# Optimization experiments

Hardware: AMD Instinct MI355X
Metric: run time of the kernel (lower is better)

Reference implementation:

```python
import jax, jax.numpy as jnp
import numpy as np

B, A, N, FIN, H, HEADS, OUT = 32, 64, 121, 12, 128, 4, 256
NL = 2          # transformer encoder layers
LEVELS = 4      # complete ternary tree: N = (3**(LEVELS+1)-1)//2 = 121
EPS = 1e-5


def setup_inputs() -> dict:
    key = jax.random.key(0)
    ks = jax.random.split(key, 10)
    s = 0.02
    # adjacency: complete ternary tree, local node indices, rows [parent, child, branch]
    child = np.arange(1, N)
    parent = (child - 1) // 3
    branch = (child - 1) % 3
    adj = np.stack([parent, child, branch], -1).astype(np.int32)  # (N-1, 3)
    adjacency = jnp.asarray(np.broadcast_to(adj, (B, A, N - 1, 3)).copy())
    perm = jax.random.permutation(ks[0], N)  # torch.randperm(n_nodes) equivalent
    forest = jax.random.normal(ks[1], (B, A, N, FIN), jnp.float32)
    p = lambda k, shape: s * jax.random.normal(k, shape, jnp.float32)
    return dict(
        forest=forest, adjacency=adjacency, perm=perm,
        w_in=p(ks[2], (H, FIN)), b_in=jnp.zeros((H,), jnp.float32),
        qkv_w=p(ks[3], (NL, 3 * H, H)), qkv_b=jnp.zeros((NL, 3 * H), jnp.float32),
        proj_w=p(ks[4], (NL, H, H)), proj_b=jnp.zeros((NL, H), jnp.float32),
        ff1_w=p(ks[5], (NL, H, H)), ff1_b=jnp.zeros((NL, H), jnp.float32),
        ff2_w=p(ks[6], (NL, H, H)), ff2_b=jnp.zeros((NL, H), jnp.float32),
        ln1_g=jnp.ones((NL, H), jnp.float32), ln1_b=jnp.zeros((NL, H), jnp.float32),
        ln2_g=jnp.ones((NL, H), jnp.float32), ln2_b=jnp.zeros((NL, H), jnp.float32),
        w_out=p(ks[7], (OUT, N * H)), b_out=jnp.zeros((OUT,), jnp.float32),
        lnf_g=jnp.ones((OUT,), jnp.float32), lnf_b=jnp.zeros((OUT,), jnp.float32))


def _ln(x, g, b):
    m = x.mean(-1, keepdims=True)
    v = ((x - m) ** 2).mean(-1, keepdims=True)  # biased var, as torch LayerNorm
    return (x - m) * jax.lax.rsqrt(v + EPS) * g + b


def _tree_pe(adjacency):
    """Level-parallel tree positional encoding: pe[child] = pe[parent] with
    bit (depth*3 + branch) set to 1 (depth 0 = first level below root)."""
    parent = adjacency[..., 0]
    branch = adjacency[..., 2]
    pe = jnp.zeros((B, A, N, H), jnp.float32)
    for l in range(1, LEVELS + 1):
        s0 = (3 ** l - 1) // 2          # first node index at level l
        e0 = (3 ** (l + 1) - 1) // 2    # one past last node at level l
        pa = parent[..., s0 - 1:e0 - 1]             # (B, A, n_l) parent local idx
        br = branch[..., s0 - 1:e0 - 1]             # (B, A, n_l) branch 0/1/2
        ppe = jnp.take_along_axis(pe, pa[..., None], axis=2)  # gather parent PE
        bits = jax.nn.one_hot((l - 1) * 3 + br, H, dtype=jnp.float32)
        pe = pe.at[:, :, s0:e0, :].set(ppe + bits)
    return pe


def _mha(x, wqkv, bqkv, wo, bo):
    S = x.shape[0]
    hd = H // HEADS
    qkv = x @ wqkv.T + bqkv
    q, k, v = [t.reshape(S, N, HEADS, hd) for t in jnp.split(qkv, 3, axis=-1)]
    logits = jnp.einsum('bqhd,bkhd->bhqk', q, k) / float(np.sqrt(hd))
    o = jnp.einsum('bhqk,bkhd->bqhd', jax.nn.softmax(logits, -1), v)
    return o.reshape(S, N, H) @ wo.T + bo


def _forward(forest, adjacency, perm, w_in, b_in, qkv_w, qkv_b, proj_w, proj_b,
             ff1_w, ff1_b, ff2_w, ff2_b, ln1_g, ln1_b, ln2_g, ln2_b,
             w_out, b_out, lnf_g, lnf_b):
    x = forest @ w_in.T + b_in + _tree_pe(adjacency)        # (B, A, N, H)
    x = x.reshape(B * A, N, H)[:, perm]                      # token shuffle
    for i in range(NL):  # post-norm encoder layers, relu FFN, dropout=0
        x = _ln(x + _mha(x, qkv_w[i], qkv_b[i], proj_w[i], proj_b[i]), ln1_g[i], ln1_b[i])
        h = jnp.maximum(x @ ff1_w[i].T + ff1_b[i], 0.0)
        x = _ln(x + h @ ff2_w[i].T + ff2_b[i], ln2_g[i], ln2_b[i])
    y = x.reshape(B * A, N * H) @ w_out.T + b_out
    return _ln(y.reshape(B, A, OUT), lnf_g, lnf_b)


def reference(forest, adjacency, perm, w_in, b_in, qkv_w, qkv_b, proj_w, proj_b,
              ff1_w, ff1_b, ff2_w, ff2_b, ln1_g, ln1_b, ln2_g, ln2_b,
              w_out, b_out, lnf_g, lnf_b):
    return _forward(forest, adjacency, perm, w_in, b_in, qkv_w, qkv_b, proj_w, proj_b,
                    ff1_w, ff1_b, ff2_w, ff2_b, ln1_g, ln1_b, ln2_g, ln2_b,
                    w_out, b_out, lnf_g, lnf_b)
```

## Files before the change

### kernel.cpp

```cpp
#include <hip/hip_runtime.h>


typedef unsigned short u16;
typedef __attribute__((ext_vector_type(8))) short bf16x8;
typedef __attribute__((ext_vector_type(4))) float f32x4;
typedef __attribute__((ext_vector_type(4))) unsigned int u32x4;

#define NTOK 121
#define HD 128
#define S_TOT 2048
#define EPSF 1e-5f

__device__ inline u16 f2bf(float f) {
  unsigned u = __float_as_uint(f);
  return (u16)((u + 0x7FFFu + ((u >> 16) & 1u)) >> 16);
}
__device__ inline float bf2f(u16 h) { return __uint_as_float(((unsigned)h) << 16); }

__device__ inline f32x4 mfma16(bf16x8 a, bf16x8 b, f32x4 c) {
  return __builtin_amdgcn_mfma_f32_16x16x32_bf16(a, b, c, 0, 0, 0);
}

__device__ inline unsigned cvt_pk_bf16(float lo, float hi) {
  unsigned r;
  asm("v_cvt_pk_bf16_f32 %0, %1, %2" : "=v"(r) : "v"(lo), "v"(hi));
  return r;
}

__device__ inline f32x4 vmax4(f32x4 a, f32x4 b) {
  f32x4 r;
  r[0] = fmaxf(a[0], b[0]); r[1] = fmaxf(a[1], b[1]);
  r[2] = fmaxf(a[2], b[2]); r[3] = fmaxf(a[3], b[3]);
  return r;
}

__device__ inline void stage16(const void* g, void* l) {
  __builtin_amdgcn_global_load_lds((__attribute__((address_space(1))) void*)g,
                                   (__attribute__((address_space(3))) void*)l,
                                   16, 0, 0);
}

__device__ inline void quad_repack(unsigned pkA, unsigned pkB, int quad,
                                   unsigned& mlo, unsigned& mhi) {
  unsigned y = (quad < 2) ? pkA : pkB;
  unsigned z = (quad < 2) ? pkB : pkA;
  unsigned a16 = (unsigned)__shfl_xor((int)y, 16);
  unsigned a32 = (unsigned)__shfl_xor((int)z, 32);
  unsigned a48 = (unsigned)__shfl_xor((int)z, 48);
  mlo = (quad == 0) ? y   : (quad == 1) ? a48 : (quad == 2) ? a32 : a16;
  mhi = (quad == 0) ? a16 : (quad == 1) ? a32 : (quad == 2) ? a48 : y;
}

__global__ __launch_bounds__(256) void convw_kernel(
    const float* __restrict__ qkvw, const float* __restrict__ projw,
    const float* __restrict__ ff1w, const float* __restrict__ ff2w,
    const float* __restrict__ wout, u16* __restrict__ dst) {
  int i = blockIdx.x * 256 + threadIdx.x;
  float v;
  if (i < 98304) v = qkvw[i];
  else if (i < 131072) v = projw[i - 98304];
  else if (i < 163840) v = ff1w[i - 131072];
  else if (i < 196608) v = ff2w[i - 163840];
  else v = wout[i - 196608];
  dst[i] = f2bf(v);
}

__global__ __launch_bounds__(256) void inproj_kernel(
    const float* __restrict__ forest, const int* __restrict__ adj,
    const int* __restrict__ perm, const float* __restrict__ WIN,
    const float* __restrict__ BIN, u16* __restrict__ X) {
  __shared__ float wf[128 * 12];
  __shared__ float fr[121 * 12];
  __shared__ float pe[121 * 12];
  __shared__ int pm[121];
  int s = blockIdx.x, tid = threadIdx.x;
  const float* fg = forest + (size_t)s * (NTOK * 12);
  const int* ag = adj + (size_t)s * (120 * 3);
  for (int i = tid; i < 128 * 12; i += 256) wf[i] = WIN[i];
  for (int i = tid; i < 121 * 12; i += 256) { fr[i] = fg[i]; pe[i] = 0.f; }
  if (tid < 121) pm[tid] = perm[tid];
  __syncthreads();
  if (tid > 0 && tid < 121) {
    int n = tid;
    int l = (n <= 3) ? 1 : (n <= 12) ? 2 : (n <= 39) ? 3 : 4;
    int cur = n;
    while (cur > 0) {
      int par = ag[(cur - 1) * 3];
      int br = ag[(cur - 1) * 3 + 2];
      pe[n * 12 + (l - 1) * 3 + br] = 1.f;
      cur = par; l--;
    }
  }
  __syncthreads();
  int h = tid & 127;
  for (int base = 0; base < 121; base += 2) {
    int i = base + (tid >> 7);
    if (i < 121) {
      int node = pm[i];
      float v = BIN[h];
#pragma unroll
      for (int k = 0; k < 12; ++k) v += fr[node * 12 + k] * wf[h * 12 + k];
      if (h < 12) v += pe[node * 12 + h];
      X[(size_t)s * (NTOK * HD) + i * HD + h] = f2bf(v);
    }
  }
}

__global__ __launch_bounds__(256, 2) void attn_kernel(
    const u16* __restrict__ X, u16* __restrict__ O,
    const u16* __restrict__ WQKV, const float* __restrict__ QKVB, int layer) {
  __shared__ u16 lds[16384];
  __shared__ u16 xl[15872];
  int tid = threadIdx.x;
  int wave = tid >> 6, lane = tid & 63, l16 = lane & 15, quad = lane >> 4;
  int seq = blockIdx.x >> 1;
  int head = ((blockIdx.x & 1) << 1) | (wave >> 1);
  int half = wave & 1;
  int hs = wave >> 1;
  u16* Kh = lds + hs * 4096;
  u16* Vh = lds + 8192 + hs * 4096;
  const u16* Xs = X + (size_t)seq * (NTOK * HD);
  const f32x4 fz = {0.f, 0.f, 0.f, 0.f};
  const int wbase = layer * 384 + head * 32;
  const u16* WQ = WQKV + (size_t)wbase * HD;
  const u16* WK = WQKV + (size_t)(wbase + 128) * HD;
  const u16* WV = WQKV + (size_t)(wbase + 256) * HD;

  {
    const char* Xb = (const char*)Xs;
#pragma unroll
    for (int j = 0; j < 8; ++j) {
      int i = wave * 8 + j;
      if (i < 31) {
        int n = i * 64 + lane;
        int r = n >> 4, c = n & 15;
        int rc = r > 120 ? 120 : r;
        stage16(Xb + rc * 256 + ((c ^ (r & 7)) << 4), (void*)(xl + i * 512));
      }
    }
  }
  bf16x8 wqf[2][4], wkf[2][4], wvf[2][4];
#pragma unroll
  for (int nt = 0; nt < 2; ++nt)
#pragma unroll
    for (int k = 0; k < 4; ++k) {
      size_t off = (size_t)(nt * 16 + l16) * HD + k * 32 + quad * 8;
      wqf[nt][k] = *(const bf16x8*)(WQ + off);
      wkf[nt][k] = *(const bf16x8*)(WK + off);
      wvf[nt][k] = *(const bf16x8*)(WV + off);
    }
  float kb2[2], vb2[2];
#pragma unroll
  for (int nt = 0; nt < 2; ++nt) {
    kb2[nt] = QKVB[wbase + 128 + nt * 16 + l16];
    vb2[nt] = QKVB[wbase + 256 + nt * 16 + l16];
  }
  const float scl = 0.17677669529663687f * 1.4426950408889634f;
  float qbias[2][4];
#pragma unroll
  for (int nt = 0; nt < 2; ++nt)
#pragma unroll
    for (int r = 0; r < 4; ++r)
      qbias[nt][r] = QKVB[wbase + nt * 16 + quad * 4 + r];
  asm volatile("s_waitcnt vmcnt(0)" ::: "memory");
  __syncthreads();

#pragma unroll 1
  for (int mt = 0; mt < 4; ++mt) {
    int tb = half * 64 + mt * 16;
    int arow = tb + l16; if (arow > 120) arow = 120;
    bf16x8 a[4];
#pragma unroll
    for (int k = 0; k < 4; ++k)
      a[k] = *(const bf16x8*)(xl + arow * 128 + (((k * 4 + quad) ^ (arow & 7)) << 3));
#pragma unroll
    for (int nt = 0; nt < 2; ++nt) {
      f32x4 kacc = fz, vacc = fz;
#pragma unroll
      for (int k = 0; k < 4; ++k) {
        kacc = mfma16(a[k], wkf[nt][k], kacc);
        vacc = mfma16(a[k], wvf[nt][k], vacc);
      }
      int d = nt * 16 + l16;
      int kc = nt * 2 + (l16 >> 3);
#pragma unroll
      for (int r = 0; r < 4; ++r) {
        int t = tb + quad * 4 + r;
        Kh[t * 32 + ((kc ^ (t & 3)) << 3) + (l16 & 7)] = f2bf(kacc[r] + kb2[nt]);
        float vv = (t < NTOK) ? (vacc[r] + vb2[nt]) : 0.f;
        Vh[d * 128 + (((t >> 3) ^ l16) << 3) + (t & 7)] = f2bf(vv);
      }
    }
  }
  __syncthreads();

#pragma unroll 1
  for (int qmt = 0; qmt < 4; ++qmt) {
    int qb = (half * 4 + qmt) * 16;
    int qrow = qb + l16;
    int qrowc = qrow > 120 ? 120 : qrow;
    bf16x8 xb[4];
#pragma unroll
    for (int k = 0; k < 4; ++k)
      xb[k] = *(const bf16x8*)(xl + qrowc * 128 + (((k * 4 + quad) ^ (qrowc & 7)) << 3));
    f32x4 qv[2];
#pragma unroll
    for (int nt = 0; nt < 2; ++nt) {
      f32x4 acc = fz;
#pragma unroll
      for (int k = 0; k < 4; ++k) acc = mfma16(wqf[nt][k], xb[k], acc);
      qv[nt] = acc;
    }
    unsigned qpk[2][2];
#pragma unroll
    for (int nt = 0; nt < 2; ++nt)
#pragma unroll
      for (int r2 = 0; r2 < 2; ++r2)
        qpk[nt][r2] = cvt_pk_bf16((qv[nt][2 * r2] + qbias[nt][2 * r2]) * scl,
                                  (qv[nt][2 * r2 + 1] + qbias[nt][2 * r2 + 1]) * scl);
    u32x4 qu;
#pragma unroll
    for (int r2 = 0; r2 < 2; ++r2) {
      unsigned mlo, mhi;
      quad_repack(qpk[0][r2], qpk[1][r2], quad, mlo, mhi);
      qu[r2] = mlo; qu[2 + r2] = mhi;
    }
    bf16x8 qfrag = __builtin_bit_cast(bf16x8, qu);
    f32x4 lg[8];
#pragma unroll
    for (int nt = 0; nt < 8; ++nt) {
      bf16x8 ka = *(const bf16x8*)(Kh + (nt * 16 + l16) * 32 + ((quad ^ (l16 & 3)) << 3));
      lg[nt] = mfma16(ka, qfrag, fz);
    }
    f32x4 t0 = vmax4(vmax4(lg[0], lg[1]), vmax4(lg[2], lg[3]));
    f32x4 t1 = vmax4(vmax4(lg[4], lg[5]), vmax4(lg[6], lg[7]));
    f32x4 tm = vmax4(t0, t1);
    float mx = fmaxf(fmaxf(tm[0], tm[1]), fmaxf(tm[2], tm[3]));
    mx = fmaxf(mx, __shfl_xor(mx, 16));
    mx = fmaxf(mx, __shfl_xor(mx, 32));
#pragma unroll
    for (int nt = 0; nt < 8; ++nt)
#pragma unroll
      for (int r = 0; r < 4; ++r) {
        float ev = __builtin_amdgcn_exp2f(lg[nt][r] - mx);
        if (nt == 7 && (quad * 4 + r > 8)) ev = 0.f;
        lg[nt][r] = ev;
      }
    f32x4 s4 = (lg[0] + lg[1]) + (lg[2] + lg[3]) + ((lg[4] + lg[5]) + (lg[6] + lg[7]));
    float sum = (s4[0] + s4[1]) + (s4[2] + s4[3]);
    sum += __shfl_xor(sum, 16);
    sum += __shfl_xor(sum, 32);
    float rinv = __builtin_amdgcn_rcpf(sum);
    unsigned pk[8][2];
#pragma unroll
    for (int nt = 0; nt < 8; ++nt)
#pragma unroll
      for (int r2 = 0; r2 < 2; ++r2)
        pk[nt][r2] = cvt_pk_bf16(lg[nt][2 * r2], lg[nt][2 * r2 + 1]);
    f32x4 oacc[2] = {fz, fz};
#pragma unroll
    for (int s = 0; s < 4; ++s) {
      u32x4 pu;
#pragma unroll
      for (int r2 = 0; r2 < 2; ++r2) {
        unsigned mlo, mhi;
        quad_repack(pk[2 * s][r2], pk[2 * s + 1][r2], quad, mlo, mhi);
        pu[r2] = mlo; pu[2 + r2] = mhi;
      }
      bf16x8 pfrag = __builtin_bit_cast(bf16x8, pu);
#pragma unroll
      for (int mt = 0; mt < 2; ++mt) {
        bf16x8 va = *(const bf16x8*)(Vh + (mt * 16 + l16) * 128 + (((s * 4 + quad) ^ l16) << 3));
        oacc[mt] = mfma16(va, pfrag, oacc[mt]);
      }
    }
    if (qrow < NTOK) {
      u16* Op = O + (size_t)seq * (NTOK * HD) + (size_t)qrow * HD + head * 32;
#pragma unroll
      for (int mt = 0; mt < 2; ++mt)
#pragma unroll
        for (int r2 = 0; r2 < 2; ++r2) {
          unsigned w = cvt_pk_bf16(oacc[mt][2 * r2] * rinv, oacc[mt][2 * r2 + 1] * rinv);
          *(unsigned*)(Op + mt * 16 + quad * 4 + 2 * r2) = w;
        }
    }
  }
}

__global__ __launch_bounds__(256) void projln_kernel(
    u16* __restrict__ X, const u16* __restrict__ O,
    const u16* __restrict__ WP, const float* __restrict__ PB,
    const float* __restrict__ G, const float* __restrict__ Bt, int layer) {
  __shared__ u16 as_[32 * 136];
  __shared__ float ct[32 * 132];
  int r0 = blockIdx.x * 32, tid = threadIdx.x;
  int wave = tid >> 6, lane = tid & 63, l16 = lane & 15, quad = lane >> 4;
  const f32x4 fz = {0.f, 0.f, 0.f, 0.f};
  for (int c = tid; c < 32 * 16; c += 256) {
    int row = c >> 4, g = c & 15;
    *(uint4*)(as_ + row * 136 + g * 8) = *(const uint4*)(O + (size_t)(r0 + row) * HD + g * 8);
  }
  __syncthreads();
  f32x4 acc[2][2] = {{fz, fz}, {fz, fz}};
#pragma unroll
  for (int k = 0; k < 4; ++k) {
    bf16x8 a0 = *(const bf16x8*)(as_ + l16 * 136 + k * 32 + quad * 8);
    bf16x8 a1 = *(const bf16x8*)(as_ + (16 + l16) * 136 + k * 32 + quad * 8);
#pragma unroll
    for (int n = 0; n < 2; ++n) {
      int nt = wave * 2 + n;
      bf16x8 bf = *(const bf16x8*)(WP + ((size_t)(layer * 128 + nt * 16 + l16)) * HD + k * 32 + quad * 8);
      acc[0][n] = mfma16(a0, bf, acc[0][n]);
      acc[1][n] = mfma16(a1, bf, acc[1][n]);
    }
  }
  for (int mt = 0; mt < 2; ++mt)
    for (int n = 0; n < 2; ++n) {
      int nt = wave * 2 + n;
#pragma unroll
      for (int r = 0; r < 4; ++r)
        ct[(mt * 16 + quad * 4 + r) * 132 + nt * 16 + l16] = acc[mt][n][r];
    }
  __syncthreads();
  int row = tid >> 3, l8 = tid & 7;
  size_t R = (size_t)(r0 + row);
  float v[16], sum = 0.f, ssq = 0.f;
#pragma unroll
  for (int i = 0; i < 16; ++i) {
    int c = l8 * 16 + i;
    float t = ct[row * 132 + c] + PB[layer * 128 + c] + bf2f(X[R * HD + c]);
    v[i] = t; sum += t; ssq += t * t;
  }
  for (int m = 1; m <= 4; m <<= 1) { sum += __shfl_xor(sum, m, 64); ssq += __shfl_xor(ssq, m, 64); }
  float mean = sum * (1.f / 128.f);
  float var = ssq * (1.f / 128.f) - mean * mean;
  float rstd = rsqrtf(var + EPSF);
#pragma unroll
  for (int i = 0; i < 16; ++i) {
    int c = l8 * 16 + i;
    X[R * HD + c] = f2bf((v[i] - mean) * rstd * G[layer * 128 + c] + Bt[layer * 128 + c]);
  }
}

__global__ __launch_bounds__(256) void ffn_kernel(
    u16* __restrict__ X,
    const u16* __restrict__ W1, const float* __restrict__ B1,
    const u16* __restrict__ W2, const float* __restrict__ B2,
    const float* __restrict__ G, const float* __restrict__ Bt, int layer) {
  __shared__ u16 as_[32 * 136];
  __shared__ u16 hs[32 * 136];
  __shared__ float ct[32 * 132];
  int r0 = blockIdx.x * 32, tid = threadIdx.x;
  int wave = tid >> 6, lane = tid & 63, l16 = lane & 15, quad = lane >> 4;
  const f32x4 fz = {0.f, 0.f, 0.f, 0.f};
  for (int c = tid; c < 32 * 16; c += 256) {
    int row = c >> 4, g = c & 15;
    *(uint4*)(as_ + row * 136 + g * 8) = *(const uint4*)(X + (size_t)(r0 + row) * HD + g * 8);
  }
  __syncthreads();
  f32x4 acc[2][2] = {{fz, fz}, {fz, fz}};
#pragma unroll
  for (int k = 0; k < 4; ++k) {
    bf16x8 a0 = *(const bf16x8*)(as_ + l16 * 136 + k * 32 + quad * 8);
    bf16x8 a1 = *(const bf16x8*)(as_ + (16 + l16) * 136 + k * 32 + quad * 8);
#pragma unroll
    for (int n = 0; n < 2; ++n) {
      int nt = wave * 2 + n;
      bf16x8 bf = *(const bf16x8*)(W1 + ((size_t)(layer * 128 + nt * 16 + l16)) * HD + k * 32 + quad * 8);
      acc[0][n] = mfma16(a0, bf, acc[0][n]);
      acc[1][n] = mfma16(a1, bf, acc[1][n]);
    }
  }
  for (int mt = 0; mt < 2; ++mt)
    for (int n = 0; n < 2; ++n) {
      int nt = wave * 2 + n;
      int col = nt * 16 + l16;
      float b1 = B1[layer * 128 + col];
#pragma unroll
      for (int r = 0; r < 4; ++r)
        hs[(mt * 16 + quad * 4 + r) * 136 + col] = f2bf(fmaxf(acc[mt][n][r] + b1, 0.f));
    }
  __syncthreads();
  f32x4 acc2[2][2] = {{fz, fz}, {fz, fz}};
#pragma unroll
  for (int k = 0; k < 4; ++k) {
    bf16x8 a0 = *(const bf16x8*)(hs + l16 * 136 + k * 32 + quad * 8);
    bf16x8 a1 = *(const bf16x8*)(hs + (16 + l16) * 136 + k * 32 + quad * 8);
#pragma unroll
    for (int n = 0; n < 2; ++n) {
      int nt = wave * 2 + n;
      bf16x8 bf = *(const bf16x8*)(W2 + ((size_t)(layer * 128 + nt * 16 + l16)) * HD + k * 32 + quad * 8);
      acc2[0][n] = mfma16(a0, bf, acc2[0][n]);
      acc2[1][n] = mfma16(a1, bf, acc2[1][n]);
    }
  }
  for (int mt = 0; mt < 2; ++mt)
    for (int n = 0; n < 2; ++n) {
      int nt = wave * 2 + n;
#pragma unroll
      for (int r = 0; r < 4; ++r)
        ct[(mt * 16 + quad * 4 + r) * 132 + nt * 16 + l16] = acc2[mt][n][r];
    }
  __syncthreads();
  int row = tid >> 3, l8 = tid & 7;
  size_t R = (size_t)(r0 + row);
  float v[16], sum = 0.f, ssq = 0.f;
#pragma unroll
  for (int i = 0; i < 16; ++i) {
    int c = l8 * 16 + i;
    float t = ct[row * 132 + c] + B2[layer * 128 + c] + bf2f(as_[row * 136 + c]);
    v[i] = t; sum += t; ssq += t * t;
  }
  for (int m = 1; m <= 4; m <<= 1) { sum += __shfl_xor(sum, m, 64); ssq += __shfl_xor(ssq, m, 64); }
  float mean = sum * (1.f / 128.f);
  float var = ssq * (1.f / 128.f) - mean * mean;
  float rstd = rsqrtf(var + EPSF);
#pragma unroll
  for (int i = 0; i < 16; ++i) {
    int c = l8 * 16 + i;
    X[R * HD + c] = f2bf((v[i] - mean) * rstd * G[layer * 128 + c] + Bt[layer * 128 + c]);
  }
}

__global__ __launch_bounds__(256, 2) void outgemm_kernel(
    const u16* __restrict__ X, const u16* __restrict__ WO, float* __restrict__ PART) {
  __shared__ u16 as_[64 * 136];
  int mtile = blockIdx.x, j = blockIdx.y;
  int tid = threadIdx.x, wave = tid >> 6, lane = tid & 63, l16 = lane & 15, quad = lane >> 4;
  int s0 = mtile * 64;
  int k0 = (j * 484) / 16, k1 = ((j + 1) * 484) / 16;
  const f32x4 fz = {0.f, 0.f, 0.f, 0.f};
  f32x4 acc[4][4];
  for (int a = 0; a < 4; ++a) for (int b = 0; b < 4; ++b) acc[a][b] = fz;
  for (int kb = k0; kb < k1; kb += 4) {
    int nst = (k1 - kb < 4) ? (k1 - kb) : 4;
    __syncthreads();
    int chunks = 64 * 4 * nst;
    for (int c = tid; c < chunks; c += 256) {
      int row = c / (4 * nst), g = c % (4 * nst);
      *(uint4*)(as_ + row * 136 + g * 8) =
          *(const uint4*)(X + (size_t)(s0 + row) * 15488 + kb * 32 + g * 8);
    }
    __syncthreads();
    for (int kk = 0; kk < nst; ++kk) {
      bf16x8 af[4];
#pragma unroll
      for (int mt = 0; mt < 4; ++mt)
        af[mt] = *(const bf16x8*)(as_ + (mt * 16 + l16) * 136 + kk * 32 + quad * 8);
#pragma unroll
      for (int n = 0; n < 4; ++n) {
        int nt = wave * 4 + n;
        bf16x8 bf = *(const bf16x8*)(WO + (size_t)(nt * 16 + l16) * 15488 +
                                     (size_t)(kb + kk) * 32 + quad * 8);
#pragma unroll
        for (int mt = 0; mt < 4; ++mt) acc[mt][n] = mfma16(af[mt], bf, acc[mt][n]);
      }
    }
  }
  for (int mt = 0; mt < 4; ++mt)
    for (int n = 0; n < 4; ++n) {
      int nt = wave * 4 + n;
#pragma unroll
      for (int r = 0; r < 4; ++r) {
        int row = s0 + mt * 16 + quad * 4 + r;
        PART[((size_t)j * 2048 + row) * 256 + nt * 16 + l16] = acc[mt][n][r];
      }
    }
}

__global__ __launch_bounds__(256) void lnf_kernel(
    const float* __restrict__ PART, const float* __restrict__ BO,
    const float* __restrict__ G, const float* __restrict__ Bt, float* __restrict__ OUT) {
  int s = blockIdx.x * 4 + (threadIdx.x >> 6);
  int lane = threadIdx.x & 63;
  float v[4], sum = 0.f, ssq = 0.f;
#pragma unroll
  for (int i = 0; i < 4; ++i) {
    int c = lane + i * 64;
    float t = BO[c];
    for (int jj = 0; jj < 16; ++jj) t += PART[((size_t)jj * 2048 + s) * 256 + c];
    v[i] = t; sum += t; ssq += t * t;
  }
  for (int m = 1; m <= 32; m <<= 1) { sum += __shfl_xor(sum, m, 64); ssq += __shfl_xor(ssq, m, 64); }
  float mean = sum * (1.f / 256.f);
  float var = ssq * (1.f / 256.f) - mean * mean;
  float rstd = rsqrtf(var + EPSF);
#pragma unroll
  for (int i = 0; i < 4; ++i) {
    int c = lane + i * 64;
    OUT[(size_t)s * 256 + c] = (v[i] - mean) * rstd * G[c] + Bt[c];
  }
}

extern "C" void kernel_launch(void* const* d_in, const int* in_sizes, int n_in,
                              void* d_out, int out_size, void* d_ws, size_t ws_size,
                              hipStream_t stream) {
  const float* forest = (const float*)d_in[0];
  const int* adj      = (const int*)d_in[1];
  const int* perm     = (const int*)d_in[2];
  const float* w_in   = (const float*)d_in[3];
  const float* b_in   = (const float*)d_in[4];
  const float* qkv_w  = (const float*)d_in[5];
  const float* qkv_b  = (const float*)d_in[6];
  const float* proj_w = (const float*)d_in[7];
  const float* proj_b = (const float*)d_in[8];
  const float* ff1_w  = (const float*)d_in[9];
  const float* ff1_b  = (const float*)d_in[10];
  const float* ff2_w  = (const float*)d_in[11];
  const float* ff2_b  = (const float*)d_in[12];
  const float* ln1_g  = (const float*)d_in[13];
  const float* ln1_b  = (const float*)d_in[14];
  const float* ln2_g  = (const float*)d_in[15];
  const float* ln2_b  = (const float*)d_in[16];
  const float* w_out  = (const float*)d_in[17];
  const float* b_out  = (const float*)d_in[18];
  const float* lnf_g  = (const float*)d_in[19];
  const float* lnf_b  = (const float*)d_in[20];

  char* ws = (char*)d_ws;
  u16* WB = (u16*)ws;
  u16* X  = (u16*)(ws + 8323072);
  u16* O  = (u16*)(ws + 8323072 + 63438848);
  float* PART = (float*)(ws + 8323072 + 2 * (size_t)63438848);

  u16* WQKV  = WB;
  u16* WPROJ = WB + 98304;
  u16* WFF1  = WB + 131072;
  u16* WFF2  = WB + 163840;
  u16* WOUT  = WB + 196608;

  convw_kernel<<<16256, 256, 0, stream>>>(qkv_w, proj_w, ff1_w, ff2_w, w_out, WB);
  inproj_kernel<<<2048, 256, 0, stream>>>(forest, adj, perm, w_in, b_in, X);
  for (int layer = 0; layer < 2; ++layer) {
    attn_kernel<<<4096, 256, 0, stream>>>(X, O, WQKV, qkv_b, layer);
    projln_kernel<<<7744, 256, 0, stream>>>(X, O, WPROJ, proj_b, ln1_g, ln1_b, layer);
    ffn_kernel<<<7744, 256, 0, stream>>>(X, WFF1, ff1_b, WFF2, ff2_b, ln2_g, ln2_b, layer);
  }
  outgemm_kernel<<<dim3(32, 16), 256, 0, stream>>>(X, WOUT, PART);
  lnf_kernel<<<512, 256, 0, stream>>>(PART, b_out, lnf_g, lnf_b, (float*)d_out);
}
```

Before: 718.5 us.

## Fuse projection+LN1 and FFN+LN2 into one register-resident block kernel

Merges the separate proj+layernorm and FFN+layernorm kernels into a single kernel handling 128 tokens per block. Each wave keeps two 16-token tiles in registers across all three GEMMs, repacking accumulators into MFMA operand fragments instead of round-tripping through shared memory or global X. This removes one launch and one global read/write of X per layer. It also adds s_setprio around MFMA groups in attention and vectorizes V and O stores. The cost is heavy register pressure from the 8x2 accumulator arrays, and weights are reloaded from global memory by every wave.

Result: faster. 689.5 us (-4.0%).

```diff
diff --git a/kernel.cpp b/kernel.cpp
--- a/kernel.cpp
+++ b/kernel.cpp
@@ -5,6 +5,7 @@
 typedef __attribute__((ext_vector_type(8))) short bf16x8;
 typedef __attribute__((ext_vector_type(4))) float f32x4;
 typedef __attribute__((ext_vector_type(4))) unsigned int u32x4;
+typedef __attribute__((ext_vector_type(2))) unsigned int u32x2;
 
 #define NTOK 121
 #define HD 128
@@ -16,6 +17,8 @@
   return (u16)((u + 0x7FFFu + ((u >> 16) & 1u)) >> 16);
 }
 __device__ inline float bf2f(u16 h) { return __uint_as_float(((unsigned)h) << 16); }
+__device__ inline float bfu32lo(unsigned u) { return __uint_as_float(u << 16); }
+__device__ inline float bfu32hi(unsigned u) { return __uint_as_float(u & 0xffff0000u); }
 
 __device__ inline f32x4 mfma16(bf16x8 a, bf16x8 b, f32x4 c) {
   return __builtin_amdgcn_mfma_f32_16x16x32_bf16(a, b, c, 0, 0, 0);
@@ -176,20 +179,28 @@
 #pragma unroll
     for (int nt = 0; nt < 2; ++nt) {
       f32x4 kacc = fz, vacc = fz;
+      __builtin_amdgcn_s_setprio(1);
 #pragma unroll
       for (int k = 0; k < 4; ++k) {
         kacc = mfma16(a[k], wkf[nt][k], kacc);
         vacc = mfma16(a[k], wvf[nt][k], vacc);
       }
+      __builtin_amdgcn_s_setprio(0);
       int d = nt * 16 + l16;
       int kc = nt * 2 + (l16 >> 3);
 #pragma unroll
       for (int r = 0; r < 4; ++r) {
         int t = tb + quad * 4 + r;
         Kh[t * 32 + ((kc ^ (t & 3)) << 3) + (l16 & 7)] = f2bf(kacc[r] + kb2[nt]);
-        float vv = (t < NTOK) ? (vacc[r] + vb2[nt]) : 0.f;
-        Vh[d * 128 + (((t >> 3) ^ l16) << 3) + (t & 7)] = f2bf(vv);
-      }
+      }
+      float vv[4];
+#pragma unroll
+      for (int r = 0; r < 4; ++r) {
+        int t = tb + quad * 4 + r;
+        vv[r] = (t < NTOK) ? (vacc[r] + vb2[nt]) : 0.f;
+      }
+      u32x2 vp = { cvt_pk_bf16(vv[0], vv[1]), cvt_pk_bf16(vv[2], vv[3]) };
+      *(u32x2*)(Vh + d * 128 + ((((tb >> 3) + (quad >> 1)) ^ l16) << 3) + (quad & 1) * 4) = vp;
     }
   }
   __syncthreads();
@@ -204,6 +215,7 @@
     for (int k = 0; k < 4; ++k)
       xb[k] = *(const bf16x8*)(xl + qrowc * 128 + (((k * 4 + quad) ^ (qrowc & 7)) << 3));
     f32x4 qv[2];
+    __builtin_amdgcn_s_setprio(1);
 #pragma unroll
     for (int nt = 0; nt < 2; ++nt) {
       f32x4 acc = fz;
@@ -211,6 +223,7 @@
       for (int k = 0; k < 4; ++k) acc = mfma16(wqf[nt][k], xb[k], acc);
       qv[nt] = acc;
     }
+    __builtin_amdgcn_s_setprio(0);
     unsigned qpk[2][2];
 #pragma unroll
     for (int nt = 0; nt < 2; ++nt)
@@ -227,11 +240,13 @@
     }
     bf16x8 qfrag = __builtin_bit_cast(bf16x8, qu);
     f32x4 lg[8];
+    __builtin_amdgcn_s_setprio(1);
 #pragma unroll
     for (int nt = 0; nt < 8; ++nt) {
       bf16x8 ka = *(const bf16x8*)(Kh + (nt * 16 + l16) * 32 + ((quad ^ (l16 & 3)) << 3));
       lg[nt] = mfma16(ka, qfrag, fz);
     }
+    __builtin_amdgcn_s_setprio(0);
     f32x4 t0 = vmax4(vmax4(lg[0], lg[1]), vmax4(lg[2], lg[3]));
     f32x4 t1 = vmax4(vmax4(lg[4], lg[5]), vmax4(lg[6], lg[7]));
     f32x4 tm = vmax4(t0, t1);
@@ -268,157 +283,227 @@
         pu[r2] = mlo; pu[2 + r2] = mhi;
       }
       bf16x8 pfrag = __builtin_bit_cast(bf16x8, pu);
+      __builtin_amdgcn_s_setprio(1);
 #pragma unroll
       for (int mt = 0; mt < 2; ++mt) {
         bf16x8 va = *(const bf16x8*)(Vh + (mt * 16 + l16) * 128 + (((s * 4 + quad) ^ l16) << 3));
         oacc[mt] = mfma16(va, pfrag, oacc[mt]);
       }
+      __builtin_amdgcn_s_setprio(0);
     }
     if (qrow < NTOK) {
       u16* Op = O + (size_t)seq * (NTOK * HD) + (size_t)qrow * HD + head * 32;
 #pragma unroll
-      for (int mt = 0; mt < 2; ++mt)
-#pragma unroll
-        for (int r2 = 0; r2 < 2; ++r2) {
-          unsigned w = cvt_pk_bf16(oacc[mt][2 * r2] * rinv, oacc[mt][2 * r2 + 1] * rinv);
-          *(unsigned*)(Op + mt * 16 + quad * 4 + 2 * r2) = w;
-        }
-    }
-  }
-}
-
-__global__ __launch_bounds__(256) void projln_kernel(
+      for (int mt = 0; mt < 2; ++mt) {
+        u32x2 w = { cvt_pk_bf16(oacc[mt][0] * rinv, oacc[mt][1] * rinv),
+                    cvt_pk_bf16(oacc[mt][2] * rinv, oacc[mt][3] * rinv) };
+        *(u32x2*)(Op + mt * 16 + quad * 4) = w;
+      }
+    }
+  }
+}
+
+__global__ __launch_bounds__(256, 2) void blockln_kernel(
     u16* __restrict__ X, const u16* __restrict__ O,
     const u16* __restrict__ WP, const float* __restrict__ PB,
-    const float* __restrict__ G, const float* __restrict__ Bt, int layer) {
-  __shared__ u16 as_[32 * 136];
-  __shared__ float ct[32 * 132];
-  int r0 = blockIdx.x * 32, tid = threadIdx.x;
+    const u16* __restrict__ W1, const float* __restrict__ B1,
+    const u16* __restrict__ W2, const float* __restrict__ B2,
+    const float* __restrict__ G1, const float* __restrict__ Bt1,
+    const float* __restrict__ G2, const float* __restrict__ Bt2, int layer) {
+  __shared__ u16 as_[128 * 128];
+  __shared__ u16 xr[128 * 128];
+  int r0 = blockIdx.x * 128, tid = threadIdx.x;
   int wave = tid >> 6, lane = tid & 63, l16 = lane & 15, quad = lane >> 4;
   const f32x4 fz = {0.f, 0.f, 0.f, 0.f};
-  for (int c = tid; c < 32 * 16; c += 256) {
-    int row = c >> 4, g = c & 15;
-    *(uint4*)(as_ + row * 136 + g * 8) = *(const uint4*)(O + (size_t)(r0 + row) * HD + g * 8);
-  }
+  const int Lb = layer * 128;
+
+  {
+    const char* Ob = (const char*)(O + (size_t)r0 * HD);
+    const char* Xb = (const char*)(X + (size_t)r0 * HD);
+#pragma unroll
+    for (int j = 0; j < 8; ++j) {
+      int n = wave * 512 + j * 64 + lane;
+      int r = n >> 4, c = n & 15;
+      int gsrc = r * 256 + ((c ^ (r & 7)) << 4);
+      stage16(Ob + gsrc, (void*)(as_ + (wave * 512 + j * 64) * 8));
+      stage16(Xb + gsrc, (void*)(xr + (wave * 512 + j * 64) * 8));
+    }
+  }
+  asm volatile("s_waitcnt vmcnt(0)" ::: "memory");
   __syncthreads();
-  f32x4 acc[2][2] = {{fz, fz}, {fz, fz}};
+
+  int tok0 = wave * 32 + l16;
+  int tok1 = wave * 32 + 16 + l16;
+
+  bf16x8 ofrag[2][4];
 #pragma unroll
   for (int k = 0; k < 4; ++k) {
-    bf16x8 a0 = *(const bf16x8*)(as_ + l16 * 136 + k * 32 + quad * 8);
-    bf16x8 a1 = *(const bf16x8*)(as_ + (16 + l16) * 136 + k * 32 + quad * 8);
-#pragma unroll
-    for (int n = 0; n < 2; ++n) {
-      int nt = wave * 2 + n;
-      bf16x8 bf = *(const bf16x8*)(WP + ((size_t)(layer * 128 + nt * 16 + l16)) * HD + k * 32 + quad * 8);
-      acc[0][n] = mfma16(a0, bf, acc[0][n]);
-      acc[1][n] = mfma16(a1, bf, acc[1][n]);
-    }
-  }
+    ofrag[0][k] = *(const bf16x8*)(as_ + tok0 * 128 + (((k * 4 + quad) ^ (tok0 & 7)) << 3));
+    ofrag[1][k] = *(const bf16x8*)(as_ + tok1 * 128 + (((k * 4 + quad) ^ (tok1 & 7)) << 3));
+  }
+
+  f32x4 acc[8][2];
+#pragma unroll
+  for (int nt = 0; nt < 8; ++nt) {
+    bf16x8 wf[4];
+#pragma unroll
+    for (int k = 0; k < 4; ++k)
+      wf[k] = *(const bf16x8*)(WP + ((size_t)(Lb + nt * 16 + l16)) * HD + k * 32 + quad * 8);
+    acc[nt][0] = fz; acc[nt][1] = fz;
+    __builtin_amdgcn_s_setprio(1);
+#pragma unroll
+    for (int k = 0; k < 4; ++k) {
+      acc[nt][0] = mfma16(wf[k], ofrag[0][k], acc[nt][0]);
+      acc[nt][1] = mfma16(wf[k], ofrag[1][k], acc[nt][1]);
+    }
+    __builtin_amdgcn_s_setprio(0);
+  }
+
+  unsigned pk1[2][8][2];
+#pragma unroll
+  for (int mt = 0; mt < 2; ++mt) {
+    int tok = (mt == 0) ? tok0 : tok1;
+    f32x4 v[8];
+    float sum = 0.f, ssq = 0.f;
+#pragma unroll
+    for (int nt = 0; nt < 8; ++nt) {
+      float4 pb4 = *(const float4*)(PB + Lb + nt * 16 + quad * 4);
+      int chunk = (nt * 2 + (quad >> 1)) ^ (tok & 7);
+      u32x2 xw = *(const u32x2*)(xr + tok * 128 + (chunk << 3) + (quad & 1) * 4);
+      v[nt][0] = acc[nt][mt][0] + pb4.x + bfu32lo(xw[0]);
+      v[nt][1] = acc[nt][mt][1] + pb4.y + bfu32hi(xw[0]);
+      v[nt][2] = acc[nt][mt][2] + pb4.z + bfu32lo(xw[1]);
+      v[nt][3] = acc[nt][mt][3] + pb4.w + bfu32hi(xw[1]);
+#pragma unroll
+      for (int r = 0; r < 4; ++r) { sum += v[nt][r]; ssq += v[nt][r] * v[nt][r]; }
+    }
+    sum += __shfl_xor(sum, 16); sum += __shfl_xor(sum, 32);
+    ssq += __shfl_xor(ssq, 16); ssq += __shfl_xor(ssq, 32);
+    float mean = sum * (1.f / 128.f);
+    float var = ssq * (1.f / 128.f) - mean * mean;
+    float rstd = rsqrtf(var + EPSF);
+#pragma unroll
+    for (int nt = 0; nt < 8; ++nt) {
+      float4 g4 = *(const float4*)(G1 + Lb + nt * 16 + quad * 4);
+      float4 b4 = *(const float4*)(Bt1 + Lb + nt * 16 + quad * 4);
+      float o0 = (v[nt][0] - mean) * rstd * g4.x + b4.x;
+      float o1 = (v[nt][1] - mean) * rstd * g4.y + b4.y;
+      float o2 = (v[nt][2] - mean) * rstd * g4.z + b4.z;
+      float o3 = (v[nt][3] - mean) * rstd * g4.w + b4.w;
+      pk1[mt][nt][0] = cvt_pk_bf16(o0, o1);
+      pk1[mt][nt][1] = cvt_pk_bf16(o2, o3);
+    }
+  }
+
+  bf16x8 pfrag[2][4];
+#pragma unroll
   for (int mt = 0; mt < 2; ++mt)
-    for (int n = 0; n < 2; ++n) {
-      int nt = wave * 2 + n;
-#pragma unroll
-      for (int r = 0; r < 4; ++r)
-        ct[(mt * 16 + quad * 4 + r) * 132 + nt * 16 + l16] = acc[mt][n][r];
-    }
-  __syncthreads();
-  int row = tid >> 3, l8 = tid & 7;
-  size_t R = (size_t)(r0 + row);
-  float v[16], sum = 0.f, ssq = 0.f;
-#pragma unroll
-  for (int i = 0; i < 16; ++i) {
-    int c = l8 * 16 + i;
-    float t = ct[row * 132 + c] + PB[layer * 128 + c] + bf2f(X[R * HD + c]);
-    v[i] = t; sum += t; ssq += t * t;
-  }
-  for (int m = 1; m <= 4; m <<= 1) { sum += __shfl_xor(sum, m, 64); ssq += __shfl_xor(ssq, m, 64); }
-  float mean = sum * (1.f / 128.f);
-  float var = ssq * (1.f / 128.f) - mean * mean;
-  float rstd = rsqrtf(var + EPSF);
-#pragma unroll
-  for (int i = 0; i < 16; ++i) {
-    int c = l8 * 16 + i;
-    X[R * HD + c] = f2bf((v[i] - mean) * rstd * G[layer * 128 + c] + Bt[layer * 128 + c]);
-  }
-}
-
-__global__ __launch_bounds__(256) void ffn_kernel(
-    u16* __restrict__ X,
-    const u16* __restrict__ W1, const float* __restrict__ B1,
-    const u16* __restrict__ W2, const float* __restrict__ B2,
-    const float* __restrict__ G, const float* __restrict__ Bt, int layer) {
-  __shared__ u16 as_[32 * 136];
-  __shared__ u16 hs[32 * 136];
-  __shared__ float ct[32 * 132];
-  int r0 = blockIdx.x * 32, tid = threadIdx.x;
-  int wave = tid >> 6, lane = tid & 63, l16 = lane & 15, quad = lane >> 4;
-  const f32x4 fz = {0.f, 0.f, 0.f, 0.f};
-  for (int c = tid; c < 32 * 16; c += 256) {
-    int row = c >> 4, g = c & 15;
-    *(uint4*)(as_ + row * 136 + g * 8) = *(const uint4*)(X + (size_t)(r0 + row) * HD + g * 8);
-  }
-  __syncthreads();
-  f32x4 acc[2][2] = {{fz, fz}, {fz, fz}};
-#pragma unroll
-  for (int k = 0; k < 4; ++k) {
-    bf16x8 a0 = *(const bf16x8*)(as_ + l16 * 136 + k * 32 + quad * 8);
-    bf16x8 a1 = *(const bf16x8*)(as_ + (16 + l16) * 136 + k * 32 + quad * 8);
-#pragma unroll
-    for (int n = 0; n < 2; ++n) {
-      int nt = wave * 2 + n;
-      bf16x8 bf = *(const bf16x8*)(W1 + ((size_t)(layer * 128 + nt * 16 + l16)) * HD + k * 32 + quad * 8);
-      acc[0][n] = mfma16(a0, bf, acc[0][n]);
-      acc[1][n] = mfma16(a1, bf, acc[1][n]);
-    }
-  }
+#pragma unroll
+    for (int s = 0; s < 4; ++s) {
+      u32x4 pu;
+#pragma unroll
+      for (int r2 = 0; r2 < 2; ++r2) {
+        unsigned mlo, mhi;
+        quad_repack(pk1[mt][2 * s][r2], pk1[mt][2 * s + 1][r2], quad, mlo, mhi);
+        pu[r2] = mlo; pu[2 + r2] = mhi;
+      }
+      pfrag[mt][s] = __builtin_bit_cast(bf16x8, pu);
+    }
+  f32x4 acc2[8][2];
+#pragma unroll
+  for (int nt = 0; nt < 8; ++nt) {
+    bf16x8 wf[4];
+#pragma unroll
+    for (int k = 0; k < 4; ++k)
+      wf[k] = *(const bf16x8*)(W1 + ((size_t)(Lb + nt * 16 + l16)) * HD + k * 32 + quad * 8);
+    acc2[nt][0] = fz; acc2[nt][1] = fz;
+    __builtin_amdgcn_s_setprio(1);
+#pragma unroll
+    for (int k = 0; k < 4; ++k) {
+      acc2[nt][0] = mfma16(wf[k], pfrag[0][k], acc2[nt][0]);
+      acc2[nt][1] = mfma16(wf[k], pfrag[1][k], acc2[nt][1]);
+    }
+    __builtin_amdgcn_s_setprio(0);
+  }
+
+  unsigned pk2[2][8][2];
+#pragma unroll
+  for (int nt = 0; nt < 8; ++nt) {
+    float4 b14 = *(const float4*)(B1 + Lb + nt * 16 + quad * 4);
+#pragma unroll
+    for (int mt = 0; mt < 2; ++mt) {
+      float h0 = fmaxf(acc2[nt][mt][0] + b14.x, 0.f);
+      float h1 = fmaxf(acc2[nt][mt][1] + b14.y, 0.f);
+      float h2 = fmaxf(acc2[nt][mt][2] + b14.z, 0.f);
+      float h3 = fmaxf(acc2[nt][mt][3] + b14.w, 0.f);
+      pk2[mt][nt][0] = cvt_pk_bf16(h0, h1);
+      pk2[mt][nt][1] = cvt_pk_bf16(h2, h3);
+    }
+  }
+  bf16x8 hfrag[2][4];
+#pragma unroll
   for (int mt = 0; mt < 2; ++mt)
-    for (int n = 0; n < 2; ++n) {
-      int nt = wave * 2 + n;
-      int col = nt * 16 + l16;
-      float b1 = B1[layer * 128 + col];
-#pragma unroll
-      for (int r = 0; r < 4; ++r)
-        hs[(mt * 16 + quad * 4 + r) * 136 + col] = f2bf(fmaxf(acc[mt][n][r] + b1, 0.f));
-    }
-  __syncthreads();
-  f32x4 acc2[2][2] = {{fz, fz}, {fz, fz}};
-#pragma unroll
-  for (int k = 0; k < 4; ++k) {
-    bf16x8 a0 = *(const bf16x8*)(hs + l16 * 136 + k * 32 + quad * 8);
-    bf16x8 a1 = *(const bf16x8*)(hs + (16 + l16) * 136 + k * 32 + quad * 8);
-#pragma unroll
-    for (int n = 0; n < 2; ++n) {
-      int nt = wave * 2 + n;
-      bf16x8 bf = *(const bf16x8*)(W2 + ((size_t)(layer * 128 + nt * 16 + l16)) * HD + k * 32 + quad * 8);
-      acc2[0][n] = mfma16(a0, bf, acc2[0][n]);
-      acc2[1][n] = mfma16(a1, bf, acc2[1][n]);
-    }
-  }
-  for (int mt = 0; mt < 2; ++mt)
-    for (int n = 0; n < 2; ++n) {
-      int nt = wave * 2 + n;
-#pragma unroll
-      for (int r = 0; r < 4; ++r)
-        ct[(mt * 16 + quad * 4 + r) * 132 + nt * 16 + l16] = acc2[mt][n][r];
-    }
-  __syncthreads();
-  int row = tid >> 3, l8 = tid & 7;
-  size_t R = (size_t)(r0 + row);
-  float v[16], sum = 0.f, ssq = 0.f;
-#pragma unroll
-  for (int i = 0; i < 16; ++i) {
-    int c = l8 * 16 + i;
-    float t = ct[row * 132 + c] + B2[layer * 128 + c] + bf2f(as_[row * 136 + c]);
-    v[i] = t; sum += t; ssq += t * t;
-  }
-  for (int m = 1; m <= 4; m <<= 1) { sum += __shfl_xor(sum, m, 64); ssq += __shfl_xor(ssq, m, 64); }
-  float mean = sum * (1.f / 128.f);
-  float var = ssq * (1.f / 128.f) - mean * mean;
-  float rstd = rsqrtf(var + EPSF);
-#pragma unroll
-  for (int i = 0; i < 16; ++i) {
-    int c = l8 * 16 + i;
-    X[R * HD + c] = f2bf((v[i] - mean) * rstd * G[layer * 128 + c] + Bt[layer * 128 + c]);
+#pragma unroll
+    for (int s = 0; s < 4; ++s) {
+      u32x4 pu;
+#pragma unroll
+      for (int r2 = 0; r2 < 2; ++r2) {
+        unsigned mlo, mhi;
+        quad_repack(pk2[mt][2 * s][r2], pk2[mt][2 * s + 1][r2], quad, mlo, mhi);
+        pu[r2] = mlo; pu[2 + r2] = mhi;
+      }
+      hfrag[mt][s] = __builtin_bit_cast(bf16x8, pu);
+    }
+
+  f32x4 acc3[8][2];
+#pragma unroll
+  for (int nt = 0; nt < 8; ++nt) {
+    bf16x8 wf[4];
+#pragma unroll
+    for (int k = 0; k < 4; ++k)
+      wf[k] = *(const bf16x8*)(W2 + ((size_t)(Lb + nt * 16 + l16)) * HD + k * 32 + quad * 8);
+    acc3[nt][0] = fz; acc3[nt][1] = fz;
+    __builtin_amdgcn_s_setprio(1);
+#pragma unroll
+    for (int k = 0; k < 4; ++k) {
+      acc3[nt][0] = mfma16(wf[k], hfrag[0][k], acc3[nt][0]);
+      acc3[nt][1] = mfma16(wf[k], hfrag[1][k], acc3[nt][1]);
+    }
+    __builtin_amdgcn_s_setprio(0);
+  }
+
+#pragma unroll
+  for (int mt = 0; mt < 2; ++mt) {
+    int tok = (mt == 0) ? tok0 : tok1;
+    f32x4 v[8];
+    float sum = 0.f, ssq = 0.f;
+#pragma unroll
+    for (int nt = 0; nt < 8; ++nt) {
+      float4 b24 = *(const float4*)(B2 + Lb + nt * 16 + quad * 4);
+      v[nt][0] = acc3[nt][mt][0] + b24.x + bfu32lo(pk1[mt][nt][0]);
+      v[nt][1] = acc3[nt][mt][1] + b24.y + bfu32hi(pk1[mt][nt][0]);
+      v[nt][2] = acc3[nt][mt][2] + b24.z + bfu32lo(pk1[mt][nt][1]);
+      v[nt][3] = acc3[nt][mt][3] + b24.w + bfu32hi(pk1[mt][nt][1]);
+#pragma unroll
+      for (int r = 0; r < 4; ++r) { sum += v[nt][r]; ssq += v[nt][r] * v[nt][r]; }
+    }
+    sum += __shfl_xor(sum, 16); sum += __shfl_xor(sum, 32);
+    ssq += __shfl_xor(ssq, 16); ssq += __shfl_xor(ssq, 32);
+    float mean = sum * (1.f / 128.f);
+    float var = ssq * (1.f / 128.f) - mean * mean;
+    float rstd = rsqrtf(var + EPSF);
+    u16* Xp = X + (size_t)(r0 + tok) * HD;
+#pragma unroll
+    for (int nt = 0; nt < 8; ++nt) {
+      float4 g4 = *(const float4*)(G2 + Lb + nt * 16 + quad * 4);
+      float4 b4 = *(const float4*)(Bt2 + Lb + nt * 16 + quad * 4);
+      float o0 = (v[nt][0] - mean) * rstd * g4.x + b4.x;
+      float o1 = (v[nt][1] - mean) * rstd * g4.y + b4.y;
+      float o2 = (v[nt][2] - mean) * rstd * g4.z + b4.z;
+      float o3 = (v[nt][3] - mean) * rstd * g4.w + b4.w;
+      u32x2 w = { cvt_pk_bf16(o0, o1), cvt_pk_bf16(o2, o3) };
+      *(u32x2*)(Xp + nt * 16 + quad * 4) = w;
+    }
   }
 }
 
@@ -533,8 +618,8 @@
   inproj_kernel<<<2048, 256, 0, stream>>>(forest, adj, perm, w_in, b_in, X);
   for (int layer = 0; layer < 2; ++layer) {
     attn_kernel<<<4096, 256, 0, stream>>>(X, O, WQKV, qkv_b, layer);
-    projln_kernel<<<7744, 256, 0, stream>>>(X, O, WPROJ, proj_b, ln1_g, ln1_b, layer);
-    ffn_kernel<<<7744, 256, 0, stream>>>(X, WFF1, ff1_b, WFF2, ff2_b, ln2_g, ln2_b, layer);
+    blockln_kernel<<<1936, 256, 0, stream>>>(X, O, WPROJ, proj_b, WFF1, ff1_b,
+                                             WFF2, ff2_b, ln1_g, ln1_b, ln2_g, ln2_b, layer);
   }
   outgemm_kernel<<<dim3(32, 16), 256, 0, stream>>>(X, WOUT, PART);
   lnf_kernel<<<512, 256, 0, stream>>>(PART, b_out, lnf_g, lnf_b, (float*)d_out);
```
